# Optimization experiments

Hardware: AMD Instinct MI355X
Metric: run time of the kernel (lower is better)

Reference implementation:

```python
import jax, jax.numpy as jnp
import numpy as np

N_EMBD = 2048
N_HEAD = 16
KV_GROUP = 4
HEAD_DIM = N_EMBD // N_HEAD          # 128
N_KV = N_HEAD // KV_GROUP            # 4
KV_DIM = N_KV * HEAD_DIM             # 512
B, T = 2, 2048
ROPE_THETA = 1000000.0


def setup_inputs() -> dict:
    key = jax.random.key(0)
    k0, k1, k2 = jax.random.split(key, 3)
    x = jax.random.normal(k0, (B, T, N_EMBD), dtype=jnp.float32)
    # weights stored (in, out); matches torch Linear math up to a transpose of random init
    W_attn = jax.random.normal(k1, (N_EMBD, N_EMBD + 2 * KV_DIM), dtype=jnp.float32) * 0.02
    b_attn = jnp.zeros((N_EMBD + 2 * KV_DIM,), dtype=jnp.float32)
    W_proj = jax.random.normal(k2, (N_EMBD, N_EMBD), dtype=jnp.float32) * 0.02
    # realistic RoPE frequencies (Qwen-style theta)
    inv_freq = 1.0 / (ROPE_THETA ** (np.arange(0, HEAD_DIM, 2, dtype=np.float64) / HEAD_DIM))
    ang = np.outer(np.arange(T, dtype=np.float64), inv_freq)  # (T, HEAD_DIM//2)
    freqs_cos = jnp.asarray(np.cos(ang), dtype=jnp.float32)
    freqs_sin = jnp.asarray(np.sin(ang), dtype=jnp.float32)
    return {"x": x, "W_attn": W_attn, "b_attn": b_attn, "W_proj": W_proj,
            "freqs_cos": freqs_cos, "freqs_sin": freqs_sin}


def _rope_expand(x, cos, sin, kv_group):
    # x: (B, T, n_kv, hd); complex rotate interleaved pairs, then expand to n_kv*kv_group heads
    Bx, Tx, nh, hd = x.shape
    xf = x.astype(jnp.float32).reshape(Bx, Tx, nh, hd // 2, 2)
    a, b = xf[..., 0], xf[..., 1]
    c = cos[None, :, None, :]  # (1, T, 1, hd//2)
    s = sin[None, :, None, :]
    yr = a * c - b * s
    yi = a * s + b * c
    y = jnp.stack([yr, yi], axis=-1).reshape(Bx, Tx, nh, hd)
    y = jnp.broadcast_to(y[:, :, :, None, :], (Bx, Tx, nh, kv_group, hd))
    return y.reshape(Bx, Tx, nh * kv_group, hd).astype(x.dtype)


def reference(x, W_attn, b_attn, W_proj, freqs_cos, freqs_sin):
    Bx, Tx, E = x.shape
    hd = 2 * freqs_cos.shape[-1]
    n_q = E // hd
    kv_dim = (W_attn.shape[1] - E) // 2
    n_kv = kv_dim // hd
    g = n_q // n_kv

    qkv = x @ W_attn + b_attn  # (B, T, E + 2*kv_dim)
    q = qkv[..., :E].reshape(Bx, Tx, n_q, hd).transpose(0, 2, 1, 3)          # bhtd
    k = qkv[..., E:E + kv_dim].reshape(Bx, Tx, n_kv, hd)
    v = qkv[..., E + kv_dim:].reshape(Bx, Tx, n_kv, hd)
    # faithful to source: RoPE on K AND V (not Q), then GQA expand
    k = _rope_expand(k, freqs_cos, freqs_sin, g).transpose(0, 2, 1, 3)       # bhtd
    v = _rope_expand(v, freqs_cos, freqs_sin, g).transpose(0, 2, 1, 3)       # bhtd

    scale = 1.0 / jnp.sqrt(jnp.asarray(hd, dtype=x.dtype))
    scores = jnp.einsum('bhqd,bhkd->bhqk', q, k) * scale                     # (B, H, T, T)
    causal = jnp.tril(jnp.ones((Tx, Tx), dtype=bool))
    scores = jnp.where(causal, scores, jnp.asarray(-jnp.inf, scores.dtype))
    attn = jax.nn.softmax(scores, axis=-1)
    y = jnp.einsum('bhqk,bhkd->bhqd', attn, v)
    y = y.transpose(0, 2, 1, 3).reshape(Bx, Tx, E)
    return y @ W_proj  # c_proj, no bias
```

## Files before the change

kernel.cpp:

```cpp
#include <hip/hip_runtime.h>
#include <cstdint>
#include <cstddef>

#define T_SEQ 2048
#define B_SZ  2
#define EMB   2048
#define NH    16
#define NKV   4
#define HD    128
#define KVD   512
#define QKVN  3072
#define MROWS (B_SZ*T_SEQ)

typedef __bf16 bf16x8 __attribute__((ext_vector_type(8)));
typedef float  f32x4  __attribute__((ext_vector_type(4)));
typedef short  s16x8  __attribute__((ext_vector_type(8)));
typedef unsigned short u16;

__device__ __forceinline__ u16 f2b(float f) {
  uint32_t u = __builtin_bit_cast(uint32_t, f);
  u += 0x7fffu + ((u >> 16) & 1u);
  return (u16)(u >> 16);
}
__device__ __forceinline__ float b2f(u16 h) {
  return __builtin_bit_cast(float, (uint32_t)h << 16);
}
__device__ __forceinline__ bf16x8 ld_bf8(const u16* p) {
  return __builtin_bit_cast(bf16x8, *(const s16x8*)p);
}
__device__ __forceinline__ void glds16(const void* g, void* l) {
  __builtin_amdgcn_global_load_lds((const __attribute__((address_space(1))) void*)g,
                                   (__attribute__((address_space(3))) void*)l, 16, 0, 0);
}
template<int N> __device__ __forceinline__ void waitv() {
  if constexpr (N == 0) asm volatile("s_waitcnt vmcnt(0)" ::: "memory");
  else if constexpr (N == 2) asm volatile("s_waitcnt vmcnt(2)" ::: "memory");
  else if constexpr (N == 3) asm volatile("s_waitcnt vmcnt(3)" ::: "memory");
  __builtin_amdgcn_sched_barrier(0);
}

__global__ void cvt_x_kernel(const float4* __restrict__ x, ushort4* __restrict__ xb, int n4) {
  int i = blockIdx.x*blockDim.x + threadIdx.x;
  if (i >= n4) return;
  float4 v = x[i];
  ushort4 o;
  o.x = f2b(v.x); o.y = f2b(v.y); o.z = f2b(v.z); o.w = f2b(v.w);
  xb[i] = o;
}

__global__ void transpose_w_kernel(const float* __restrict__ in, u16* __restrict__ out,
                                   int R, int C) {
  __shared__ float tile[64][65];
  int c0 = blockIdx.x*64, r0 = blockIdx.y*64;
  int tx = threadIdx.x, ty = threadIdx.y;
#pragma unroll
  for (int k = 0; k < 4; ++k) {
    int r = ty + k*16;
    float4 v = *(const float4*)&in[(size_t)(r0+r)*C + c0 + tx*4];
    tile[r][tx*4+0] = v.x; tile[r][tx*4+1] = v.y;
    tile[r][tx*4+2] = v.z; tile[r][tx*4+3] = v.w;
  }
  __syncthreads();
#pragma unroll
  for (int k = 0; k < 4; ++k) {
    int c = ty + k*16;
    ushort4 o;
    o.x = f2b(tile[tx*4+0][c]);
    o.y = f2b(tile[tx*4+1][c]);
    o.z = f2b(tile[tx*4+2][c]);
    o.w = f2b(tile[tx*4+3][c]);
    *(ushort4*)&out[(size_t)(c0+c)*R + r0 + tx*4] = o;
  }
}

template<int BN, int WGN, int MF, int NF, int NF1, int SB, int SB1, int VMC, bool BF16_OUT>
__global__ __launch_bounds__(512, 2) void gemm_kernel(const u16* __restrict__ A,
        const u16* __restrict__ Bt, const float* __restrict__ bias,
        void* __restrict__ Cout, int M, int N, int K) {
  constexpr int MF2 = MF/2;
  __shared__ u16 As[2][256*64];
  __shared__ u16 Bs[2][BN*64];
  const int tid = threadIdx.x;
  const int w = tid >> 6, lane = tid & 63;
  const int quad = lane >> 4, lc = lane & 15;
  const int wrow = w / WGN, wcol = w % WGN;
  const int gx = gridDim.x;
  const int lin = blockIdx.y*gx + blockIdx.x;
  const int swz = (lin & 7)*32 + (lin >> 3);
  const int m0 = (swz / gx)*256, n0 = (swz % gx)*BN;

  f32x4 acc[MF][NF] = {};
  bf16x8 af[MF2][2], bfv[NF][2];

  int xoff[2];
#pragma unroll
  for (int ks = 0; ks < 2; ++ks) xoff[ks] = ((ks*4 + quad) ^ (lc & 7))*8;
  const int arow0 = (wrow*MF*16 + lc)*64;
  const int brow0 = (wcol*NF*16 + lc)*64;

  const int srb  = tid >> 3;
  const int spos = (tid & 7) ^ (srb & 7);
  const u16* sAp = A  + (size_t)(m0 + srb)*K + spos*8;
  const u16* sBp = Bt + (size_t)(n0 + srb)*K + spos*8;

#define STAGE_A(bf_, t_, h_) do { \
    glds16(sAp + (size_t)((h_)*2  )*64*K + (size_t)(t_)*64, &As[bf_][((h_)*2  )*4096 + w*512]); \
    glds16(sAp + (size_t)((h_)*2+1)*64*K + (size_t)(t_)*64, &As[bf_][((h_)*2+1)*4096 + w*512]); \
  } while (0)
#define STAGE_B(bf_, t_, p_) do { \
    _Pragma("unroll") for (int r = (p_) ? SB1 : 0; r < ((p_) ? SB : SB1); ++r) \
      glds16(sBp + (size_t)r*64*K + (size_t)(t_)*64, &Bs[bf_][r*4096 + w*512]); \
  } while (0)
#define LDAH(S_, h_) do { _Pragma("unroll") for (int i = 0; i < MF2; ++i) { \
    af[i][0] = ld_bf8((S_) + arow0 + ((h_)*MF2 + i)*1024 + xoff[0]); \
    af[i][1] = ld_bf8((S_) + arow0 + ((h_)*MF2 + i)*1024 + xoff[1]); } } while (0)
#define LDBG(S_, g_) do { _Pragma("unroll") for (int j = (g_) ? NF1 : 0; j < ((g_) ? NF : NF1); ++j) { \
    bfv[j][0] = ld_bf8((S_) + brow0 + j*1024 + xoff[0]); \
    bfv[j][1] = ld_bf8((S_) + brow0 + j*1024 + xoff[1]); } } while (0)
#define CL(h_, g_) do { _Pragma("unroll") for (int ks = 0; ks < 2; ++ks) \
    _Pragma("unroll") for (int i = 0; i < MF2; ++i) \
    _Pragma("unroll") for (int j = (g_) ? NF1 : 0; j < ((g_) ? NF : NF1); ++j) \
      acc[(h_)*MF2+i][j] = __builtin_amdgcn_mfma_f32_16x16x32_bf16( \
          af[i][ks], bfv[j][ks], acc[(h_)*MF2+i][j], 0, 0, 0); } while (0)
#define BARX()  __builtin_amdgcn_s_barrier()
#define SCHB()  __builtin_amdgcn_sched_barrier(0)
#define MFMAPH(h_, g_) do { BARX(); \
    asm volatile("s_waitcnt lgkmcnt(0)" ::: "memory"); SCHB(); \
    __builtin_amdgcn_s_setprio(1); CL(h_, g_); __builtin_amdgcn_s_setprio(0); \
  } while (0)

  const int NT = K >> 6;
  STAGE_B(0, 0, 0); STAGE_B(0, 0, 1);
  STAGE_A(0, 0, 0); STAGE_A(0, 0, 1);
  STAGE_B(1, 1, 0); STAGE_B(1, 1, 1);
  waitv<VMC>();
  BARX(); SCHB();

  for (int t0 = 0; t0 < NT-2; t0 += 2) {
    const u16 *a0 = As[0], *b0 = Bs[0], *a1 = As[1], *b1 = Bs[1];
    LDAH(a0, 0); LDBG(b0, 0); STAGE_A(1, t0+1, 0);
    MFMAPH(0, 0); BARX();
    LDBG(b0, 1); STAGE_A(1, t0+1, 1);
    MFMAPH(0, 1); BARX();
    LDAH(a0, 1); STAGE_B(0, t0+2, 0);
    MFMAPH(1, 0); BARX();
    STAGE_B(0, t0+2, 1);
    MFMAPH(1, 1);
    waitv<VMC>();
    BARX(); SCHB();
    LDAH(a1, 0); LDBG(b1, 0); STAGE_A(0, t0+2, 0);
    MFMAPH(0, 0); BARX();
    LDBG(b1, 1); STAGE_A(0, t0+2, 1);
    MFMAPH(0, 1); BARX();
    LDAH(a1, 1); STAGE_B(1, t0+3, 0);
    MFMAPH(1, 0); BARX();
    STAGE_B(1, t0+3, 1);
    MFMAPH(1, 1);
    waitv<VMC>();
    BARX(); SCHB();
  }
  {
    const u16 *a0 = As[0], *b0 = Bs[0], *a1 = As[1], *b1 = Bs[1];
    LDAH(a0, 0); LDBG(b0, 0); STAGE_A(1, NT-1, 0);
    MFMAPH(0, 0); BARX();
    LDBG(b0, 1); STAGE_A(1, NT-1, 1);
    MFMAPH(0, 1); BARX();
    LDAH(a0, 1);
    MFMAPH(1, 0); BARX();
    MFMAPH(1, 1);
    waitv<0>();
    BARX(); SCHB();
    LDAH(a1, 0); LDBG(b1, 0);
    MFMAPH(0, 0); BARX();
    LDBG(b1, 1);
    MFMAPH(0, 1); BARX();
    LDAH(a1, 1);
    MFMAPH(1, 0); BARX();
    MFMAPH(1, 1);
  }

#undef STAGE_A
#undef STAGE_B
#undef LDAH
#undef LDBG
#undef CL
#undef BARX
#undef SCHB
#undef MFMAPH

#pragma unroll
  for (int j = 0; j < NF; ++j) {
    int col = n0 + wcol*NF*16 + j*16 + lc;
    float bv = BF16_OUT ? bias[col] : 0.0f;
#pragma unroll
    for (int i = 0; i < MF; ++i) {
      int rowb = m0 + wrow*MF*16 + i*16 + quad*4;
#pragma unroll
      for (int r = 0; r < 4; ++r) {
        float v = acc[i][j][r] + bv;
        if (BF16_OUT) ((u16*)Cout)[(size_t)(rowb+r)*N + col] = f2b(v);
        else          ((float*)Cout)[(size_t)(rowb+r)*N + col] = v;
      }
    }
  }
}

__global__ void rope_kernel(const u16* __restrict__ qkv, const float* __restrict__ fc,
                            const float* __restrict__ fs, u16* __restrict__ kout,
                            u16* __restrict__ vout) {
  int tid = threadIdx.x;
  int row = blockIdx.x;
  int i = tid & 63, kv = tid >> 6;
  int t = row & (T_SEQ-1);
  const u16* p = qkv + (size_t)row*QKVN + EMB + kv*HD + 2*i;
  float ka = b2f(p[0]),   kb = b2f(p[1]);
  float va = b2f(p[KVD]), vb = b2f(p[KVD+1]);
  float c = fc[t*64+i], s = fs[t*64+i];
  size_t ob = (size_t)row*KVD + kv*HD + 2*i;
  kout[ob]   = f2b(ka*c - kb*s);
  kout[ob+1] = f2b(ka*s + kb*c);
  vout[ob]   = f2b(va*c - vb*s);
  vout[ob+1] = f2b(va*s + vb*c);
}

__global__ void transpose_v_kernel(const u16* __restrict__ vb, u16* __restrict__ vtb) {
  __shared__ u16 tile[32][33];
  int bkv = blockIdx.z;
  int b = bkv >> 2, kv = bkv & 3;
  int d0 = blockIdx.y*32, t0 = blockIdx.x*32;
  int tx = threadIdx.x, ty = threadIdx.y;
#pragma unroll
  for (int i = 0; i < 32; i += 8)
    tile[ty+i][tx] = vb[(size_t)(b*T_SEQ + t0+ty+i)*KVD + kv*HD + d0 + tx];
  __syncthreads();
#pragma unroll
  for (int i = 0; i < 32; i += 8)
    vtb[(size_t)(bkv*HD + d0+ty+i)*T_SEQ + t0 + tx] = tile[tx][ty+i];
}

__global__ __launch_bounds__(256, 2) void flash_kernel(const u16* __restrict__ qkv,
    const u16* __restrict__ kb, const u16* __restrict__ vtb, u16* __restrict__ yb) {
  __shared__ u16 Ks[2][64*128];
  __shared__ u16 Vs[2][128*64];
  __shared__ u16 Ps[4][16*64];
  const int tid = threadIdx.x;
  const int w = tid >> 6, lane = tid & 63;
  const int quad = lane >> 4, lc = lane & 15;
  const int bkv = blockIdx.x & 7;
  const int r_  = blockIdx.x >> 3;
  const int b = bkv >> 2, kv = bkv & 3;
  const int h = kv*4 + w;
  const int qbA = r_*16;
  const int qbB = (127 - r_)*16;

  bf16x8 qfA[4], qfB[4];
  {
    const u16* qpA = qkv + (size_t)(b*T_SEQ + qbA + lc)*QKVN + h*HD + quad*8;
    const u16* qpB = qkv + (size_t)(b*T_SEQ + qbB + lc)*QKVN + h*HD + quad*8;
#pragma unroll
    for (int ks = 0; ks < 4; ++ks) { qfA[ks] = ld_bf8(qpA + ks*32); qfB[ks] = ld_bf8(qpB + ks*32); }
  }

  f32x4 oA[8] = {}, oB[8] = {};
  float rsA[4] = {0.f,0.f,0.f,0.f}, rsB[4] = {0.f,0.f,0.f,0.f};
  const u16* kbase = kb  + (size_t)b*T_SEQ*KVD + kv*HD;
  const u16* vbase = vtb + (size_t)bkv*HD*T_SEQ;
  const int ntA = (qbA + 16 + 63) >> 6;
  const int nt  = (qbB + 16 + 63) >> 6;
  const float cs = 0.08838834764831845f * 1.4426950408889634f;
  u16* pw = Ps[w];

  const u16* kptr[4];
  const u16* vptr[4];
#pragma unroll
  for (int rr = 0; rr < 4; ++rr) {
    int krow = (rr*4 + w)*4 + (lane >> 4);
    int kcc  = (lane & 15) ^ (krow & 15);
    kptr[rr] = kbase + (size_t)krow*KVD + kcc*8;
    int vrow = (rr*4 + w)*8 + (lane >> 3);
    int vcc  = (lane & 7) ^ (vrow & 7);
    vptr[rr] = vbase + (size_t)vrow*T_SEQ + vcc*8;
  }

  int koff[4], voff[2], poff[2];
#pragma unroll
  for (int ks = 0; ks < 4; ++ks) koff[ks] = lc*128 + (((ks*4 + quad) ^ lc)*8);
#pragma unroll
  for (int ks = 0; ks < 2; ++ks) voff[ks] = lc*64 + (((ks*4 + quad) ^ (lc & 7))*8);
#pragma unroll
  for (int ks = 0; ks < 2; ++ks) poff[ks] = lc*64 + (((ks*4 + quad) ^ (lc & 7))*8);
  int pwb[4], pwx[4];
#pragma unroll
  for (int r = 0; r < 4; ++r) {
    pwb[r] = (quad*4 + r)*64 + (lc & 7);
    pwx[r] = (quad*4 + r) & 7;
  }
  const int pcc = lc >> 3;

#pragma unroll
  for (int rr = 0; rr < 4; ++rr) glds16(kptr[rr], &Ks[0][(rr*4 + w)*512]);
#pragma unroll
  for (int rr = 0; rr < 4; ++rr) glds16(vptr[rr], &Vs[0][(rr*4 + w)*512]);
  asm volatile("s_waitcnt vmcnt(0)" ::: "memory");
  __builtin_amdgcn_sched_barrier(0);
  __builtin_amdgcn_s_barrier();
  __builtin_amdgcn_sched_barrier(0);

#define SMAX(SC_, QB_, RS_) do { \
    if (k0 + 63 > (QB_)) { \
      _Pragma("unroll") for (int nt2 = 0; nt2 < 4; ++nt2) { \
        int key = k0 + nt2*16 + lc; \
        int qrow = (QB_) + quad*4; \
        _Pragma("unroll") for (int r = 0; r < 4; ++r) { \
          float e = __builtin_amdgcn_exp2f(SC_[nt2][r]*cs); \
          float p = (key <= qrow + r) ? e : 0.0f; \
          RS_[r] += p; \
          pw[pwb[r] + ((nt2*2 + pcc) ^ pwx[r])*8] = f2b(p); \
        } \
      } \
    } else { \
      _Pragma("unroll") for (int nt2 = 0; nt2 < 4; ++nt2) \
        _Pragma("unroll") for (int r = 0; r < 4; ++r) { \
          float p = __builtin_amdgcn_exp2f(SC_[nt2][r]*cs); \
          RS_[r] += p; \
          pw[pwb[r] + ((nt2*2 + pcc) ^ pwx[r])*8] = f2b(p); \
        } \
    } \
  } while (0)

#define TILE_BODY(DOA_) do { \
    f32x4 scB[4] = {}; f32x4 scA[4] = {}; \
    __builtin_amdgcn_s_setprio(1); \
    _Pragma("unroll") for (int nt2 = 0; nt2 < 4; ++nt2) { \
      bf16x8 kf[4]; \
      _Pragma("unroll") for (int ks = 0; ks < 4; ++ks) \
        kf[ks] = ld_bf8(ksb + nt2*16*128 + koff[ks]); \
      _Pragma("unroll") for (int ks = 0; ks < 4; ++ks) { \
        scB[nt2] = __builtin_amdgcn_mfma_f32_16x16x32_bf16(qfB[ks], kf[ks], scB[nt2], 0, 0, 0); \
        if (DOA_) scA[nt2] = __builtin_amdgcn_mfma_f32_16x16x32_bf16(qfA[ks], kf[ks], scA[nt2], 0, 0, 0); \
      } \
    } \
    __builtin_amdgcn_s_setprio(0); \
    SMAX(scB, qbB, rsB); \
    bf16x8 paB[2]; \
    _Pragma("unroll") for (int ks = 0; ks < 2; ++ks) paB[ks] = ld_bf8(pw + poff[ks]); \
    bf16x8 paA[2]; \
    if (DOA_) { \
      SMAX(scA, qbA, rsA); \
      _Pragma("unroll") for (int ks = 0; ks < 2; ++ks) paA[ks] = ld_bf8(pw + poff[ks]); \
    } \
    __builtin_amdgcn_s_setprio(1); \
    _Pragma("unroll") for (int j = 0; j < 8; ++j) { \
      bf16x8 vf0 = ld_bf8(vsb + j*16*64 + voff[0]); \
      bf16x8 vf1 = ld_bf8(vsb + j*16*64 + voff[1]); \
      oB[j] = __builtin_amdgcn_mfma_f32_16x16x32_bf16(paB[0], vf0, oB[j], 0, 0, 0); \
      oB[j] = __builtin_amdgcn_mfma_f32_16x16x32_bf16(paB[1], vf1, oB[j], 0, 0, 0); \
      if (DOA_) { \
        oA[j] = __builtin_amdgcn_mfma_f32_16x16x32_bf16(paA[0], vf0, oA[j], 0, 0, 0); \
        oA[j] = __builtin_amdgcn_mfma_f32_16x16x32_bf16(paA[1], vf1, oA[j], 0, 0, 0); \
      } \
    } \
    __builtin_amdgcn_s_setprio(0); \
  } while (0)

  for (int t = 0; t < nt; ++t) {
    const int cur = t & 1;
    if (t + 1 < nt) {
#pragma unroll
      for (int rr = 0; rr < 4; ++rr)
        glds16(kptr[rr] + (size_t)(t+1)*64*KVD, &Ks[cur^1][(rr*4 + w)*512]);
#pragma unroll
      for (int rr = 0; rr < 4; ++rr)
        glds16(vptr[rr] + (size_t)(t+1)*64,     &Vs[cur^1][(rr*4 + w)*512]);
    }
    const u16* ksb = Ks[cur];
    const u16* vsb = Vs[cur];
    const int k0 = t*64;

    if (t < ntA) { TILE_BODY(1); } else { TILE_BODY(0); }

    asm volatile("s_waitcnt vmcnt(0)" ::: "memory");
    __builtin_amdgcn_sched_barrier(0);
    __builtin_amdgcn_s_barrier();
    __builtin_amdgcn_sched_barrier(0);
  }
#undef TILE_BODY
#undef SMAX

#pragma unroll
  for (int r = 0; r < 4; ++r) {
    float vA = rsA[r], vB = rsB[r];
#pragma unroll
    for (int off2 = 8; off2 >= 1; off2 >>= 1) {
      vA += __shfl_xor(vA, off2);
      vB += __shfl_xor(vB, off2);
    }
    float invA = 1.0f / vA, invB = 1.0f / vB;
    size_t orowA = (size_t)(b*T_SEQ + qbA + quad*4 + r)*EMB + h*HD;
    size_t orowB = (size_t)(b*T_SEQ + qbB + quad*4 + r)*EMB + h*HD;
#pragma unroll
    for (int j = 0; j < 8; ++j) {
      yb[orowA + j*16 + lc] = f2b(oA[j][r]*invA);
      yb[orowB + j*16 + lc] = f2b(oB[j][r]*invB);
    }
  }
}

extern "C" void kernel_launch(void* const* d_in, const int* in_sizes, int n_in,
                              void* d_out, int out_size, void* d_ws, size_t ws_size,
                              hipStream_t stream) {
  const float* x      = (const float*)d_in[0];
  const float* W_attn = (const float*)d_in[1];
  const float* b_attn = (const float*)d_in[2];
  const float* W_proj = (const float*)d_in[3];
  const float* fc     = (const float*)d_in[4];
  const float* fs     = (const float*)d_in[5];

  u16* ws   = (u16*)d_ws;
  u16* xb   = ws;
  u16* WaT  = xb   + (size_t)MROWS*EMB;
  u16* qkv  = WaT  + (size_t)QKVN*EMB;
  u16* kbuf = qkv  + (size_t)MROWS*QKVN;
  u16* vb   = kbuf + (size_t)MROWS*KVD;
  u16* vtb  = vb   + (size_t)MROWS*KVD;
  u16* WpT  = WaT;
  u16* yb   = xb;
  float* out = (float*)d_out;

  cvt_x_kernel<<<(MROWS*EMB/4 + 255)/256, 256, 0, stream>>>(
      (const float4*)x, (ushort4*)xb, MROWS*EMB/4);
  transpose_w_kernel<<<dim3(QKVN/64, EMB/64), dim3(16, 16), 0, stream>>>(
      W_attn, WaT, EMB, QKVN);
  gemm_kernel<192, 4, 8, 3, 2, 3, 2, 3, true>
      <<<dim3(QKVN/192, MROWS/256), 512, 0, stream>>>(
      xb, WaT, b_attn, qkv, MROWS, QKVN, EMB);
  rope_kernel<<<MROWS, 256, 0, stream>>>(qkv, fc, fs, kbuf, vb);
  transpose_v_kernel<<<dim3(T_SEQ/32, HD/32, B_SZ*NKV), dim3(32, 8), 0, stream>>>(vb, vtb);
  transpose_w_kernel<<<dim3(EMB/64, EMB/64), dim3(16, 16), 0, stream>>>(
      W_proj, WpT, EMB, EMB);
  flash_kernel<<<dim3(B_SZ*NKV*(T_SEQ/32)), 256, 0, stream>>>(qkv, kbuf, vtb, yb);
  gemm_kernel<128, 2, 4, 4, 2, 2, 1, 2, false>
      <<<dim3(EMB/128, MROWS/256), 512, 0, stream>>>(
      yb, WpT, nullptr, out, MROWS, EMB, EMB);
}
```

Baseline: 279.7 us.

## Pair adjacent query blocks per workgroup instead of mirrored causal pairing

Each workgroup now handles two adjacent 16-row query blocks that share every K/V tile, instead of pairing block r with block 127-r. Because both halves always use each loaded tile, the separate single-half path is gone and the A and B MMAs run unconditionally. This cuts total tile iterations, barriers and K/V loads, but per-workgroup work now varies widely with query position. A heaviest-first dispatch order is meant to soften that imbalance, yet the longest workgroups now do paired MMAs on every tile.

```diff
diff --git a/kernel.cpp b/kernel.cpp
--- a/kernel.cpp
+++ b/kernel.cpp
@@ -247,11 +247,12 @@
   const int w = tid >> 6, lane = tid & 63;
   const int quad = lane >> 4, lc = lane & 15;
   const int bkv = blockIdx.x & 7;
-  const int r_  = blockIdx.x >> 3;
+  const int g_  = blockIdx.x >> 3;
+  const int gg  = (g_ < 32) ? (63 - 2*g_) : (2*(g_ - 32));
   const int b = bkv >> 2, kv = bkv & 3;
   const int h = kv*4 + w;
-  const int qbA = r_*16;
-  const int qbB = (127 - r_)*16;
+  const int qbA = gg*32;
+  const int qbB = gg*32 + 16;
 
   bf16x8 qfA[4], qfB[4];
   {
@@ -265,8 +266,7 @@
   float rsA[4] = {0.f,0.f,0.f,0.f}, rsB[4] = {0.f,0.f,0.f,0.f};
   const u16* kbase = kb  + (size_t)b*T_SEQ*KVD + kv*HD;
   const u16* vbase = vtb + (size_t)bkv*HD*T_SEQ;
-  const int ntA = (qbA + 16 + 63) >> 6;
-  const int nt  = (qbB + 16 + 63) >> 6;
+  const int nt = (qbB + 16 + 63) >> 6;
   const float cs = 0.08838834764831845f * 1.4426950408889634f;
   u16* pw = Ps[w];
 
@@ -328,41 +328,6 @@
     } \
   } while (0)
 
-#define TILE_BODY(DOA_) do { \
-    f32x4 scB[4] = {}; f32x4 scA[4] = {}; \
-    __builtin_amdgcn_s_setprio(1); \
-    _Pragma("unroll") for (int nt2 = 0; nt2 < 4; ++nt2) { \
-      bf16x8 kf[4]; \
-      _Pragma("unroll") for (int ks = 0; ks < 4; ++ks) \
-        kf[ks] = ld_bf8(ksb + nt2*16*128 + koff[ks]); \
-      _Pragma("unroll") for (int ks = 0; ks < 4; ++ks) { \
-        scB[nt2] = __builtin_amdgcn_mfma_f32_16x16x32_bf16(qfB[ks], kf[ks], scB[nt2], 0, 0, 0); \
-        if (DOA_) scA[nt2] = __builtin_amdgcn_mfma_f32_16x16x32_bf16(qfA[ks], kf[ks], scA[nt2], 0, 0, 0); \
-      } \
-    } \
-    __builtin_amdgcn_s_setprio(0); \
-    SMAX(scB, qbB, rsB); \
-    bf16x8 paB[2]; \
-    _Pragma("unroll") for (int ks = 0; ks < 2; ++ks) paB[ks] = ld_bf8(pw + poff[ks]); \
-    bf16x8 paA[2]; \
-    if (DOA_) { \
-      SMAX(scA, qbA, rsA); \
-      _Pragma("unroll") for (int ks = 0; ks < 2; ++ks) paA[ks] = ld_bf8(pw + poff[ks]); \
-    } \
-    __builtin_amdgcn_s_setprio(1); \
-    _Pragma("unroll") for (int j = 0; j < 8; ++j) { \
-      bf16x8 vf0 = ld_bf8(vsb + j*16*64 + voff[0]); \
-      bf16x8 vf1 = ld_bf8(vsb + j*16*64 + voff[1]); \
-      oB[j] = __builtin_amdgcn_mfma_f32_16x16x32_bf16(paB[0], vf0, oB[j], 0, 0, 0); \
-      oB[j] = __builtin_amdgcn_mfma_f32_16x16x32_bf16(paB[1], vf1, oB[j], 0, 0, 0); \
-      if (DOA_) { \
-        oA[j] = __builtin_amdgcn_mfma_f32_16x16x32_bf16(paA[0], vf0, oA[j], 0, 0, 0); \
-        oA[j] = __builtin_amdgcn_mfma_f32_16x16x32_bf16(paA[1], vf1, oA[j], 0, 0, 0); \
-      } \
-    } \
-    __builtin_amdgcn_s_setprio(0); \
-  } while (0)
-
   for (int t = 0; t < nt; ++t) {
     const int cur = t & 1;
     if (t + 1 < nt) {
@@ -377,14 +342,48 @@
     const u16* vsb = Vs[cur];
     const int k0 = t*64;
 
-    if (t < ntA) { TILE_BODY(1); } else { TILE_BODY(0); }
+    f32x4 scA[4] = {}, scB[4] = {};
+    __builtin_amdgcn_s_setprio(1);
+#pragma unroll
+    for (int nt2 = 0; nt2 < 4; ++nt2) {
+      bf16x8 kf[4];
+#pragma unroll
+      for (int ks = 0; ks < 4; ++ks)
+        kf[ks] = ld_bf8(ksb + nt2*16*128 + koff[ks]);
+#pragma unroll
+      for (int ks = 0; ks < 4; ++ks) {
+        scB[nt2] = __builtin_amdgcn_mfma_f32_16x16x32_bf16(qfB[ks], kf[ks], scB[nt2], 0, 0, 0);
+        scA[nt2] = __builtin_amdgcn_mfma_f32_16x16x32_bf16(qfA[ks], kf[ks], scA[nt2], 0, 0, 0);
+      }
+    }
+    __builtin_amdgcn_s_setprio(0);
+
+    SMAX(scB, qbB, rsB);
+    bf16x8 paB[2];
+#pragma unroll
+    for (int ks = 0; ks < 2; ++ks) paB[ks] = ld_bf8(pw + poff[ks]);
+    SMAX(scA, qbA, rsA);
+    bf16x8 paA[2];
+#pragma unroll
+    for (int ks = 0; ks < 2; ++ks) paA[ks] = ld_bf8(pw + poff[ks]);
+
+    __builtin_amdgcn_s_setprio(1);
+#pragma unroll
+    for (int j = 0; j < 8; ++j) {
+      bf16x8 vf0 = ld_bf8(vsb + j*16*64 + voff[0]);
+      bf16x8 vf1 = ld_bf8(vsb + j*16*64 + voff[1]);
+      oB[j] = __builtin_amdgcn_mfma_f32_16x16x32_bf16(paB[0], vf0, oB[j], 0, 0, 0);
+      oB[j] = __builtin_amdgcn_mfma_f32_16x16x32_bf16(paB[1], vf1, oB[j], 0, 0, 0);
+      oA[j] = __builtin_amdgcn_mfma_f32_16x16x32_bf16(paA[0], vf0, oA[j], 0, 0, 0);
+      oA[j] = __builtin_amdgcn_mfma_f32_16x16x32_bf16(paA[1], vf1, oA[j], 0, 0, 0);
+    }
+    __builtin_amdgcn_s_setprio(0);
 
     asm volatile("s_waitcnt vmcnt(0)" ::: "memory");
     __builtin_amdgcn_sched_barrier(0);
     __builtin_amdgcn_s_barrier();
     __builtin_amdgcn_sched_barrier(0);
   }
-#undef TILE_BODY
 #undef SMAX
 
 #pragma unroll
```

Result: slower. 289.5 us (+3.5%).
